# Optimization experiments

Hardware: AMD Instinct MI355X
Metric: run time of the kernel (lower is better)

Reference implementation:

```python
import jax, jax.numpy as jnp
import numpy as np

N_NODES = 50000
N_EDGES = 1600000
D = 128
N_GRAPHS = 512


def _glorot(key, shape):
    fan_in, fan_out = shape[1], shape[0]
    lim = float(np.sqrt(6.0 / (fan_in + fan_out)))
    return jax.random.uniform(key, shape, jnp.float32, -lim, lim)


def setup_inputs() -> dict:
    key = jax.random.key(0)
    ks = jax.random.split(key, 16)
    inp = {
        "x": jax.random.normal(ks[0], (N_NODES, D), jnp.float32),
        "edge_index": jax.random.randint(ks[1], (2, N_EDGES), 0, N_NODES, jnp.int64),
        "batch": jnp.sort(jax.random.randint(ks[2], (N_NODES,), 0, N_GRAPHS, jnp.int64)),
    }
    # 3 SAGEConv layers: W_l (neighbor path, with bias), W_r (root path, no bias)
    for l in range(3):
        inp[f"Wl{l}"] = _glorot(ks[3 + 3 * l], (D, D))
        inp[f"b{l}"] = jnp.zeros((D,), jnp.float32)
        inp[f"Wr{l}"] = _glorot(ks[4 + 3 * l], (D, D))
    inp["fc_w"] = _glorot(ks[14], (1, D))
    inp["fc_b"] = jnp.zeros((1,), jnp.float32)
    return inp


def _sage_layer(x, src, dst, Wl, b, Wr):
    # mean aggregation of source features at destination nodes
    deg = jax.ops.segment_sum(jnp.ones((src.shape[0],), x.dtype), dst, num_segments=N_NODES)
    agg = jax.ops.segment_sum(x[src], dst, num_segments=N_NODES)  # [N, D] gather+scatter
    agg = agg / jnp.clip(deg, 1.0)[:, None]
    return agg @ Wl.T + b + x @ Wr.T


def reference(x, edge_index, batch, Wl0, b0, Wr0, Wl1, b1, Wr1, Wl2, b2, Wr2, fc_w, fc_b):
    src, dst = edge_index[0], edge_index[1]
    for Wl, b, Wr in ((Wl0, b0, Wr0), (Wl1, b1, Wr1), (Wl2, b2, Wr2)):
        x = jax.nn.relu(_sage_layer(x, src, dst, Wl, b, Wr))  # dropout p=0 -> identity
    # global mean pool per graph
    cnt = jax.ops.segment_sum(jnp.ones((x.shape[0],), x.dtype), batch, num_segments=N_GRAPHS)
    pooled = jax.ops.segment_sum(x, batch, num_segments=N_GRAPHS) / jnp.clip(cnt, 1.0)[:, None]
    return pooled @ fc_w.T + fc_b
```

## Files before the change

### kernel.cpp

```cpp
#include <hip/hip_runtime.h>

#define N_NODES  50000
#define N_EDGES  1600000
#define DIM      128
#define N_GRAPHS 512
#define SCAN_BLOCK 1024
#define NB1   196
#define B1    256
#define CHUNK 6250
#define BH_N  (NB1 * B1)
#define BH_BLK ((BH_N + SCAN_BLOCK - 1) / SCAN_BLOCK)
#define XS_BLOCKS 6250
#define WS_BLOCKS 384
#define GB_BLOCKS 196

typedef unsigned int uint_t;
typedef unsigned short ushort_t;
typedef __attribute__((ext_vector_type(8))) short bf16x8;
typedef __attribute__((ext_vector_type(4))) float f32x4;

__device__ inline uint_t bf_rne(float f) {
    uint_t u = __float_as_uint(f);
    return (u + 0x7fffu + ((u >> 16) & 1u)) >> 16;
}

__device__ inline void bf_split(float f, uint_t& h, uint_t& l) {
    h = bf_rne(f);
    float hf = __uint_as_float(h << 16);
    l = bf_rne(f - hf);
}

__global__ __launch_bounds__(256) void prep_kernel(
        const int* __restrict__ dst, int* __restrict__ bh,
        const float* __restrict__ x, ushort_t* __restrict__ xh, ushort_t* __restrict__ xl,
        const float* w0, const float* w1, const float* w2,
        const float* w3, const float* w4, const float* w5,
        ushort_t* __restrict__ whi,
        const int* __restrict__ batch, int* __restrict__ gstart) {
    __shared__ int hist[NB1];
    int b = blockIdx.x, t = threadIdx.x;
    if (b < B1) {
        for (int i = t; i < NB1; i += 256) hist[i] = 0;
        __syncthreads();
        int base = b * CHUNK;
        for (int i = t; i < CHUNK; i += 256)
            atomicAdd(&hist[dst[base + i] >> 8], 1);
        __syncthreads();
        for (int i = t; i < NB1; i += 256) bh[i * B1 + b] = hist[i];
    } else if (b < B1 + XS_BLOCKS) {
        int i = (b - B1) * 256 + t;
        float4 v = ((const float4*)x)[i];
        uint_t h0,h1,h2,h3,l0,l1,l2,l3;
        bf_split(v.x,h0,l0); bf_split(v.y,h1,l1); bf_split(v.z,h2,l2); bf_split(v.w,h3,l3);
        uint2 ho; ho.x = h0 | (h1 << 16); ho.y = h2 | (h3 << 16);
        uint2 lo; lo.x = l0 | (l1 << 16); lo.y = l2 | (l3 << 16);
        ((uint2*)xh)[i] = ho;
        ((uint2*)xl)[i] = lo;
    } else if (b < B1 + XS_BLOCKS + WS_BLOCKS) {
        int i = (b - B1 - XS_BLOCKS) * 256 + t;
        int ws = i >> 14, off = i & 16383;
        const float* w = (ws == 0) ? w0 : (ws == 1) ? w1 : (ws == 2) ? w2
                       : (ws == 3) ? w3 : (ws == 4) ? w4 : w5;
        whi[i] = (ushort_t)bf_rne(w[off]);
    } else {
        int i = (b - B1 - XS_BLOCKS - WS_BLOCKS) * 256 + t;
        if (i < N_NODES) {
            int bb = batch[i];
            int prev = (i == 0) ? -1 : batch[i - 1];
            for (int g = prev + 1; g <= bb; g++) gstart[g] = i;
            if (i == 0) {
                int last = batch[N_NODES - 1];
                for (int g = last + 1; g <= N_GRAPHS; g++) gstart[g] = N_NODES;
            }
        }
    }
}

__global__ void block_reduce_n(const int* __restrict__ in, int* __restrict__ bsum, int n) {
    __shared__ int red[256];
    int b = blockIdx.x, t = threadIdx.x;
    int base = b * SCAN_BLOCK;
    int s = 0;
    for (int i = t; i < SCAN_BLOCK; i += 256) {
        int idx = base + i;
        s += (idx < n) ? in[idx] : 0;
    }
    red[t] = s; __syncthreads();
    for (int off = 128; off; off >>= 1) {
        if (t < off) red[t] += red[t + off];
        __syncthreads();
    }
    if (t == 0) bsum[b] = red[0];
}

__global__ void scan_tops_n(const int* __restrict__ bsum, int* __restrict__ bofs, int nblk) {
    if (threadIdx.x == 0) {
        int acc = 0;
        for (int i = 0; i < nblk; i++) { bofs[i] = acc; acc += bsum[i]; }
    }
}

__global__ void block_scan_n(const int* __restrict__ in, const int* __restrict__ bofs,
                             int* __restrict__ ofs, int n) {
    __shared__ int tmp[SCAN_BLOCK];
    int b = blockIdx.x, t = threadIdx.x;
    int i = b * SCAN_BLOCK + t;
    tmp[t] = (i < n) ? in[i] : 0;
    __syncthreads();
    for (int off = 1; off < SCAN_BLOCK; off <<= 1) {
        int add = (t >= off) ? tmp[t - off] : 0;
        __syncthreads();
        tmp[t] += add;
        __syncthreads();
    }
    if (i < n) ofs[i + 1] = tmp[t] + bofs[b];
    if (i == 0) ofs[0] = 0;
}

__global__ __launch_bounds__(256) void p1_scatter(const int* __restrict__ src,
                                                  const int* __restrict__ dst,
                                                  const int* __restrict__ bhofs,
                                                  uint_t* __restrict__ ebuf1) {
    __shared__ int cur[NB1];
    int b = blockIdx.x, t = threadIdx.x;
    for (int i = t; i < NB1; i += 256) cur[i] = bhofs[i * B1 + b];
    __syncthreads();
    int base = b * CHUNK;
    for (int i = t; i < CHUNK; i += 256) {
        int d = dst[base + i];
        int pos = atomicAdd(&cur[d >> 8], 1);
        ebuf1[pos] = (uint_t)src[base + i] | ((uint_t)(d & 255) << 16);
    }
}

__global__ __launch_bounds__(256) void p2_sort(const uint_t* __restrict__ ebuf1,
                                               const int* __restrict__ bhofs,
                                               int* __restrict__ row_start,
                                               int* __restrict__ ebuf) {
    __shared__ int hist[256];
    __shared__ int scn[256];
    __shared__ int cur[256];
    int k = blockIdx.x, t = threadIdx.x;
    int s = bhofs[k * B1];
    int e = (k == NB1 - 1) ? N_EDGES : bhofs[(k + 1) * B1];
    hist[t] = 0;
    __syncthreads();
    for (int i = s + t; i < e; i += 256)
        atomicAdd(&hist[(ebuf1[i] >> 16) & 255], 1);
    __syncthreads();
    int v = hist[t];
    scn[t] = v;
    __syncthreads();
    for (int off = 1; off < 256; off <<= 1) {
        int add = (t >= off) ? scn[t - off] : 0;
        __syncthreads();
        scn[t] += add;
        __syncthreads();
    }
    int ex = scn[t] - v;
    int node = k * 256 + t;
    if (node < N_NODES) row_start[node] = s + ex;
    if (k == NB1 - 1 && t == 0) row_start[N_NODES] = N_EDGES;
    cur[t] = s + ex;
    __syncthreads();
    for (int i = s + t; i < e; i += 256) {
        uint_t p = ebuf1[i];
        int pos = atomicAdd(&cur[(p >> 16) & 255], 1);
        ebuf[pos] = (int)(p & 0xffffu);
    }
}

__global__ __launch_bounds__(256) void agg_kernel(const ushort_t* __restrict__ xb,
                                                  const int* __restrict__ row_start,
                                                  const int* __restrict__ ebuf,
                                                  ushort_t* __restrict__ agg_hi,
                                                  ushort_t* __restrict__ agg_lo) {
    int node = blockIdx.x * 4 + (threadIdx.x >> 6);
    if (node >= N_NODES) return;
    int lane = threadIdx.x & 63;
    int grp = lane >> 4, fl = lane & 15;
    int s = row_start[node], e = row_start[node + 1];
    float a0=0.f,a1=0.f,a2=0.f,a3=0.f,a4=0.f,a5=0.f,a6=0.f,a7=0.f;
    const uint4* x8 = (const uint4*)xb;
    for (int i = s; i < e; i += 64) {
        int nloc = e - i; if (nloc > 64) nloc = 64;
        int src_l = (i + lane < e) ? ebuf[i + lane] : 0;
        int jmax = (nloc + 3) & ~3;
        #pragma unroll 4
        for (int j = 0; j < jmax; j += 4) {
            int slot = j + grp;
            int src = __shfl(src_l, slot & 63, 64);
            if (slot < nloc) {
                uint4 v = x8[(size_t)src * 16 + fl];
                a0 += __uint_as_float(v.x << 16);
                a1 += __uint_as_float(v.x & 0xffff0000u);
                a2 += __uint_as_float(v.y << 16);
                a3 += __uint_as_float(v.y & 0xffff0000u);
                a4 += __uint_as_float(v.z << 16);
                a5 += __uint_as_float(v.z & 0xffff0000u);
                a6 += __uint_as_float(v.w << 16);
                a7 += __uint_as_float(v.w & 0xffff0000u);
            }
        }
    }
    a0 += __shfl_xor(a0, 16, 64); a0 += __shfl_xor(a0, 32, 64);
    a1 += __shfl_xor(a1, 16, 64); a1 += __shfl_xor(a1, 32, 64);
    a2 += __shfl_xor(a2, 16, 64); a2 += __shfl_xor(a2, 32, 64);
    a3 += __shfl_xor(a3, 16, 64); a3 += __shfl_xor(a3, 32, 64);
    a4 += __shfl_xor(a4, 16, 64); a4 += __shfl_xor(a4, 32, 64);
    a5 += __shfl_xor(a5, 16, 64); a5 += __shfl_xor(a5, 32, 64);
    a6 += __shfl_xor(a6, 16, 64); a6 += __shfl_xor(a6, 32, 64);
    a7 += __shfl_xor(a7, 16, 64); a7 += __shfl_xor(a7, 32, 64);
    if (grp == 0) {
        float inv = (e > s) ? 1.0f / (float)(e - s) : 0.0f;
        float v[8] = {a0*inv,a1*inv,a2*inv,a3*inv,a4*inv,a5*inv,a6*inv,a7*inv};
        uint_t h[8], l[8];
        #pragma unroll
        for (int k = 0; k < 8; k++) bf_split(v[k], h[k], l[k]);
        uint4 ho, lo;
        ho.x = h[0] | (h[1] << 16); ho.y = h[2] | (h[3] << 16);
        ho.z = h[4] | (h[5] << 16); ho.w = h[6] | (h[7] << 16);
        lo.x = l[0] | (l[1] << 16); lo.y = l[2] | (l[3] << 16);
        lo.z = l[4] | (l[5] << 16); lo.w = l[6] | (l[7] << 16);
        ((uint4*)agg_hi)[(size_t)node * 16 + fl] = ho;
        ((uint4*)agg_lo)[(size_t)node * 16 + fl] = lo;
    }
}

__global__ __launch_bounds__(256, 2) void sage_gemm_mfma(
        const ushort_t* __restrict__ agg_hi, const ushort_t* __restrict__ agg_lo,
        const ushort_t* __restrict__ x_hi,   const ushort_t* __restrict__ x_lo,
        const ushort_t* __restrict__ wl_hi,  const ushort_t* __restrict__ wr_hi,
        const float* __restrict__ bias,
        ushort_t* __restrict__ out_hi, ushort_t* __restrict__ out_lo, int nrows) {
    __shared__ ushort_t whi_s[2][16384];
    int t = threadIdx.x;
    for (int i = t; i < 4096; i += 256) {
        int a = i >> 11, rem = i & 2047, row = rem >> 4, ch = rem & 15;
        int sw = ch ^ (row & 7);
        const ushort_t* srcp = a ? wr_hi : wl_hi;
        uint4 v = *(const uint4*)(srcp + row * DIM + ch * 8);
        *(uint4*)((char*)&whi_s[a][0] + row * 256 + sw * 16) = v;
    }
    __syncthreads();

    int wave = t >> 6, lane = t & 63;
    int ml = lane & 15, quad = lane >> 4;
    int m0 = blockIdx.x * 64 + wave * 16;
    int row = m0 + ml;
    int rowc = (row < nrows) ? row : (nrows - 1);
    size_t abase = (size_t)rowc * DIM + quad * 8;

    f32x4 acc[8];
    #pragma unroll
    for (int i = 0; i < 8; i++) acc[i] = (f32x4)0.f;

    #pragma unroll
    for (int kc = 0; kc < DIM; kc += 32) {
        bf16x8 Aah = *(const bf16x8*)(agg_hi + abase + kc);
        bf16x8 Aal = *(const bf16x8*)(agg_lo + abase + kc);
        bf16x8 Axh = *(const bf16x8*)(x_hi   + abase + kc);
        bf16x8 Axl = *(const bf16x8*)(x_lo   + abase + kc);
        int kch = (kc >> 3) + quad;
        int sw16 = (kch ^ (ml & 7)) * 16;
        #pragma unroll
        for (int n0 = 0; n0 < 8; n0++) {
            int nrow = n0 * 16 + ml;
            bf16x8 b_lh = *(const bf16x8*)((const char*)&whi_s[0][0] + nrow * 256 + sw16);
            bf16x8 b_rh = *(const bf16x8*)((const char*)&whi_s[1][0] + nrow * 256 + sw16);
            f32x4 c = acc[n0];
            c = __builtin_amdgcn_mfma_f32_16x16x32_bf16(Aah, b_lh, c, 0, 0, 0);
            c = __builtin_amdgcn_mfma_f32_16x16x32_bf16(Aal, b_lh, c, 0, 0, 0);
            c = __builtin_amdgcn_mfma_f32_16x16x32_bf16(Axh, b_rh, c, 0, 0, 0);
            c = __builtin_amdgcn_mfma_f32_16x16x32_bf16(Axl, b_rh, c, 0, 0, 0);
            acc[n0] = c;
        }
    }

    #pragma unroll
    for (int n0 = 0; n0 < 8; n0++) {
        int col = n0 * 16 + ml;
        float bv = bias[col];
        #pragma unroll
        for (int r = 0; r < 4; r++) {
            int orow = m0 + quad * 4 + r;
            if (orow < nrows) {
                float v = fmaxf(acc[n0][r] + bv, 0.f);
                uint_t h, l;
                bf_split(v, h, l);
                out_hi[(size_t)orow * DIM + col] = (ushort_t)h;
                out_lo[(size_t)orow * DIM + col] = (ushort_t)l;
            }
        }
    }
}

__global__ __launch_bounds__(256) void pool_fc(const ushort_t* __restrict__ x_hi,
                                               const ushort_t* __restrict__ x_lo,
                                               const int* __restrict__ gstart,
                                               const float* __restrict__ fc_w,
                                               const float* __restrict__ fc_b,
                                               float* __restrict__ out) {
    int g = blockIdx.x * 4 + (threadIdx.x >> 6);
    if (g >= N_GRAPHS) return;
    int lane = threadIdx.x & 63;
    int s = gstart[g], e = gstart[g + 1];
    float ax = 0.f, ay = 0.f;
    const uint_t* xh = (const uint_t*)x_hi;
    const uint_t* xl = (const uint_t*)x_lo;
    for (int i = s; i < e; i++) {
        uint_t h = xh[(size_t)i * 64 + lane];
        uint_t l = xl[(size_t)i * 64 + lane];
        ax += __uint_as_float(h << 16) + __uint_as_float(l << 16);
        ay += __uint_as_float(h & 0xffff0000u) + __uint_as_float(l & 0xffff0000u);
    }
    float inv = (e > s) ? 1.0f / (float)(e - s) : 0.0f;
    const float2* w2 = (const float2*)fc_w;
    float2 w = w2[lane];
    float sres = (ax * w.x + ay * w.y) * inv;
    for (int off = 32; off; off >>= 1) sres += __shfl_down(sres, off, 64);
    if (lane == 0) out[g] = sres + fc_b[0];
}

extern "C" void kernel_launch(void* const* d_in, const int* in_sizes, int n_in,
                              void* d_out, int out_size, void* d_ws, size_t ws_size,
                              hipStream_t stream) {
    const float* x     = (const float*)d_in[0];
    const int*   ei    = (const int*)d_in[1];
    const int*   batch = (const int*)d_in[2];
    const float* Wl[3] = {(const float*)d_in[3], (const float*)d_in[6], (const float*)d_in[9]};
    const float* bb[3] = {(const float*)d_in[4], (const float*)d_in[7], (const float*)d_in[10]};
    const float* Wr[3] = {(const float*)d_in[5], (const float*)d_in[8], (const float*)d_in[11]};
    const float* fc_w  = (const float*)d_in[12];
    const float* fc_b  = (const float*)d_in[13];
    float* out = (float*)d_out;

    char* p = (char*)d_ws;
    auto alloc = [&](size_t bytes) { char* r = p; p += (bytes + 255) & ~255ull; return r; };
    int* bh        = (int*)alloc((size_t)BH_N * 4);
    int* bhofs     = (int*)alloc((size_t)(BH_N + 1) * 4);
    int* bsum      = (int*)alloc((size_t)BH_BLK * 4);
    int* bofs      = (int*)alloc((size_t)BH_BLK * 4);
    uint_t* ebuf1  = (uint_t*)alloc((size_t)N_EDGES * 4);
    int* ebuf      = (int*)alloc((size_t)N_EDGES * 4);
    int* row_start = (int*)alloc((size_t)(N_NODES + 1) * 4);
    int* gstart    = (int*)alloc((size_t)(N_GRAPHS + 1) * 4);
    const size_t FB = (size_t)N_NODES * DIM * 2;
    ushort_t* agg_hi = (ushort_t*)alloc(FB);
    ushort_t* agg_lo = (ushort_t*)alloc(FB);
    ushort_t* fh[3]  = {(ushort_t*)alloc(FB), (ushort_t*)alloc(FB), (ushort_t*)alloc(FB)};
    ushort_t* fl_[3] = {(ushort_t*)alloc(FB), (ushort_t*)alloc(FB), (ushort_t*)alloc(FB)};
    ushort_t* whi    = (ushort_t*)alloc((size_t)6 * 16384 * 2);

    const int* src = ei;
    const int* dst = ei + N_EDGES;

    prep_kernel<<<B1 + XS_BLOCKS + WS_BLOCKS + GB_BLOCKS, 256, 0, stream>>>(
        dst, bh, x, fh[0], fl_[0], Wl[0], Wr[0], Wl[1], Wr[1], Wl[2], Wr[2],
        whi, batch, gstart);
    block_reduce_n<<<BH_BLK, 256, 0, stream>>>(bh, bsum, BH_N);
    scan_tops_n<<<1, 64, 0, stream>>>(bsum, bofs, BH_BLK);
    block_scan_n<<<BH_BLK, SCAN_BLOCK, 0, stream>>>(bh, bofs, bhofs, BH_N);
    p1_scatter<<<B1, 256, 0, stream>>>(src, dst, bhofs, ebuf1);
    p2_sort<<<NB1, 256, 0, stream>>>(ebuf1, bhofs, row_start, ebuf);

    int inb = 0;
    for (int l = 0; l < 3; l++) {
        int outb = (l == 0) ? 1 : (l == 1) ? 2 : 1;
        agg_kernel<<<(N_NODES + 3) / 4, 256, 0, stream>>>(fh[inb], row_start, ebuf, agg_hi, agg_lo);
        sage_gemm_mfma<<<(N_NODES + 63) / 64, 256, 0, stream>>>(
            agg_hi, agg_lo, fh[inb], fl_[inb],
            whi + (size_t)(2 * l) * 16384, whi + (size_t)(2 * l + 1) * 16384,
            bb[l], fh[outb], fl_[outb], N_NODES);
        inb = outb;
    }
    pool_fc<<<(N_GRAPHS + 3) / 4, 256, 0, stream>>>(fh[inb], fl_[inb], gstart, fc_w, fc_b, out);
}
```

Baseline: 442.5 us.

## Fuse global mean pool and FC into last GEMM epilogue; merge scan kernels

The last SAGE layer's GEMM epilogue now does bias, ReLU and the dot product with fc_w, reduces across lanes, and atomically adds each row's contribution divided by its graph size into the output. The output is pre-initialised with fc_b in the prep kernel. This removes the final feature-map write and the separate pool_fc kernel. The single-thread top-level scan is also folded into the block scan kernel via a wave shuffle scan, which removes one launch. The cost is atomic contention on 512 outputs and a summation order that is no longer deterministic.

```diff
diff --git a/kernel.cpp b/kernel.cpp
--- a/kernel.cpp
+++ b/kernel.cpp
@@ -13,6 +13,7 @@
 #define XS_BLOCKS 6250
 #define WS_BLOCKS 384
 #define GB_BLOCKS 196
+#define OI_BLOCKS 2
 
 typedef unsigned int uint_t;
 typedef unsigned short ushort_t;
@@ -36,7 +37,8 @@
         const float* w0, const float* w1, const float* w2,
         const float* w3, const float* w4, const float* w5,
         ushort_t* __restrict__ whi,
-        const int* __restrict__ batch, int* __restrict__ gstart) {
+        const int* __restrict__ batch, int* __restrict__ gstart,
+        const float* __restrict__ fc_b, float* __restrict__ out) {
     __shared__ int hist[NB1];
     int b = blockIdx.x, t = threadIdx.x;
     if (b < B1) {
@@ -62,7 +64,7 @@
         const float* w = (ws == 0) ? w0 : (ws == 1) ? w1 : (ws == 2) ? w2
                        : (ws == 3) ? w3 : (ws == 4) ? w4 : w5;
         whi[i] = (ushort_t)bf_rne(w[off]);
-    } else {
+    } else if (b < B1 + XS_BLOCKS + WS_BLOCKS + GB_BLOCKS) {
         int i = (b - B1 - XS_BLOCKS - WS_BLOCKS) * 256 + t;
         if (i < N_NODES) {
             int bb = batch[i];
@@ -73,6 +75,9 @@
                 for (int g = last + 1; g <= N_GRAPHS; g++) gstart[g] = N_NODES;
             }
         }
+    } else {
+        int i = (b - B1 - XS_BLOCKS - WS_BLOCKS - GB_BLOCKS) * 256 + t;
+        if (i < N_GRAPHS) out[i] = fc_b[0];
     }
 }
 
@@ -93,17 +98,21 @@
     if (t == 0) bsum[b] = red[0];
 }
 
-__global__ void scan_tops_n(const int* __restrict__ bsum, int* __restrict__ bofs, int nblk) {
-    if (threadIdx.x == 0) {
-        int acc = 0;
-        for (int i = 0; i < nblk; i++) { bofs[i] = acc; acc += bsum[i]; }
-    }
-}
-
-__global__ void block_scan_n(const int* __restrict__ in, const int* __restrict__ bofs,
-                             int* __restrict__ ofs, int n) {
+__global__ void scan_finalize(const int* __restrict__ in, const int* __restrict__ bsum,
+                              int* __restrict__ ofs, int n, int nblk) {
+    __shared__ int small[64];
     __shared__ int tmp[SCAN_BLOCK];
     int b = blockIdx.x, t = threadIdx.x;
+    if (t < 64) {
+        int v = (t < nblk) ? bsum[t] : 0;
+        for (int off = 1; off < 64; off <<= 1) {
+            int u = __shfl_up(v, off, 64);
+            if (t >= off) v += u;
+        }
+        small[t] = v;
+    }
+    __syncthreads();
+    int base = (b == 0) ? 0 : small[b - 1];
     int i = b * SCAN_BLOCK + t;
     tmp[t] = (i < n) ? in[i] : 0;
     __syncthreads();
@@ -113,7 +122,7 @@
         tmp[t] += add;
         __syncthreads();
     }
-    if (i < n) ofs[i + 1] = tmp[t] + bofs[b];
+    if (i < n) ofs[i + 1] = tmp[t] + base;
     if (i == 0) ofs[0] = 0;
 }
 
@@ -232,7 +241,9 @@
         const ushort_t* __restrict__ x_hi,   const ushort_t* __restrict__ x_lo,
         const ushort_t* __restrict__ wl_hi,  const ushort_t* __restrict__ wr_hi,
         const float* __restrict__ bias,
-        ushort_t* __restrict__ out_hi, ushort_t* __restrict__ out_lo, int nrows) {
+        ushort_t* __restrict__ out_hi, ushort_t* __restrict__ out_lo,
+        const int* __restrict__ batch, const int* __restrict__ gstart,
+        const float* __restrict__ fc_w, float* __restrict__ pool_out, int nrows) {
     __shared__ ushort_t whi_s[2][16384];
     int t = threadIdx.x;
     for (int i = t; i < 4096; i += 256) {
@@ -277,49 +288,47 @@
         }
     }
 
-    #pragma unroll
-    for (int n0 = 0; n0 < 8; n0++) {
-        int col = n0 * 16 + ml;
-        float bv = bias[col];
+    if (pool_out) {
+        float rd[4] = {0.f, 0.f, 0.f, 0.f};
+        #pragma unroll
+        for (int n0 = 0; n0 < 8; n0++) {
+            int col = n0 * 16 + ml;
+            float bv = bias[col];
+            float w  = fc_w[col];
+            #pragma unroll
+            for (int r = 0; r < 4; r++)
+                rd[r] += fmaxf(acc[n0][r] + bv, 0.f) * w;
+        }
         #pragma unroll
         for (int r = 0; r < 4; r++) {
+            #pragma unroll
+            for (int off = 1; off < 16; off <<= 1)
+                rd[r] += __shfl_xor(rd[r], off, 64);
             int orow = m0 + quad * 4 + r;
-            if (orow < nrows) {
-                float v = fmaxf(acc[n0][r] + bv, 0.f);
-                uint_t h, l;
-                bf_split(v, h, l);
-                out_hi[(size_t)orow * DIM + col] = (ushort_t)h;
-                out_lo[(size_t)orow * DIM + col] = (ushort_t)l;
+            if (orow < nrows && ml == 0) {
+                int g = batch[orow];
+                float cnt = (float)(gstart[g + 1] - gstart[g]);
+                atomicAdd(&pool_out[g], rd[r] / cnt);
             }
         }
-    }
-}
-
-__global__ __launch_bounds__(256) void pool_fc(const ushort_t* __restrict__ x_hi,
-                                               const ushort_t* __restrict__ x_lo,
-                                               const int* __restrict__ gstart,
-                                               const float* __restrict__ fc_w,
-                                               const float* __restrict__ fc_b,
-                                               float* __restrict__ out) {
-    int g = blockIdx.x * 4 + (threadIdx.x >> 6);
-    if (g >= N_GRAPHS) return;
-    int lane = threadIdx.x & 63;
-    int s = gstart[g], e = gstart[g + 1];
-    float ax = 0.f, ay = 0.f;
-    const uint_t* xh = (const uint_t*)x_hi;
-    const uint_t* xl = (const uint_t*)x_lo;
-    for (int i = s; i < e; i++) {
-        uint_t h = xh[(size_t)i * 64 + lane];
-        uint_t l = xl[(size_t)i * 64 + lane];
-        ax += __uint_as_float(h << 16) + __uint_as_float(l << 16);
-        ay += __uint_as_float(h & 0xffff0000u) + __uint_as_float(l & 0xffff0000u);
-    }
-    float inv = (e > s) ? 1.0f / (float)(e - s) : 0.0f;
-    const float2* w2 = (const float2*)fc_w;
-    float2 w = w2[lane];
-    float sres = (ax * w.x + ay * w.y) * inv;
-    for (int off = 32; off; off >>= 1) sres += __shfl_down(sres, off, 64);
-    if (lane == 0) out[g] = sres + fc_b[0];
+    } else {
+        #pragma unroll
+        for (int n0 = 0; n0 < 8; n0++) {
+            int col = n0 * 16 + ml;
+            float bv = bias[col];
+            #pragma unroll
+            for (int r = 0; r < 4; r++) {
+                int orow = m0 + quad * 4 + r;
+                if (orow < nrows) {
+                    float v = fmaxf(acc[n0][r] + bv, 0.f);
+                    uint_t h, l;
+                    bf_split(v, h, l);
+                    out_hi[(size_t)orow * DIM + col] = (ushort_t)h;
+                    out_lo[(size_t)orow * DIM + col] = (ushort_t)l;
+                }
+            }
+        }
+    }
 }
 
 extern "C" void kernel_launch(void* const* d_in, const int* in_sizes, int n_in,
@@ -340,7 +349,6 @@
     int* bh        = (int*)alloc((size_t)BH_N * 4);
     int* bhofs     = (int*)alloc((size_t)(BH_N + 1) * 4);
     int* bsum      = (int*)alloc((size_t)BH_BLK * 4);
-    int* bofs      = (int*)alloc((size_t)BH_BLK * 4);
     uint_t* ebuf1  = (uint_t*)alloc((size_t)N_EDGES * 4);
     int* ebuf      = (int*)alloc((size_t)N_EDGES * 4);
     int* row_start = (int*)alloc((size_t)(N_NODES + 1) * 4);
@@ -355,24 +363,23 @@
     const int* src = ei;
     const int* dst = ei + N_EDGES;
 
-    prep_kernel<<<B1 + XS_BLOCKS + WS_BLOCKS + GB_BLOCKS, 256, 0, stream>>>(
+    prep_kernel<<<B1 + XS_BLOCKS + WS_BLOCKS + GB_BLOCKS + OI_BLOCKS, 256, 0, stream>>>(
         dst, bh, x, fh[0], fl_[0], Wl[0], Wr[0], Wl[1], Wr[1], Wl[2], Wr[2],
-        whi, batch, gstart);
+        whi, batch, gstart, fc_b, out);
     block_reduce_n<<<BH_BLK, 256, 0, stream>>>(bh, bsum, BH_N);
-    scan_tops_n<<<1, 64, 0, stream>>>(bsum, bofs, BH_BLK);
-    block_scan_n<<<BH_BLK, SCAN_BLOCK, 0, stream>>>(bh, bofs, bhofs, BH_N);
+    scan_finalize<<<BH_BLK, SCAN_BLOCK, 0, stream>>>(bh, bsum, bhofs, BH_N, BH_BLK);
     p1_scatter<<<B1, 256, 0, stream>>>(src, dst, bhofs, ebuf1);
     p2_sort<<<NB1, 256, 0, stream>>>(ebuf1, bhofs, row_start, ebuf);
 
     int inb = 0;
     for (int l = 0; l < 3; l++) {
-        int outb = (l == 0) ? 1 : (l == 1) ? 2 : 1;
+        int outb = (l == 0) ? 1 : 2;
         agg_kernel<<<(N_NODES + 3) / 4, 256, 0, stream>>>(fh[inb], row_start, ebuf, agg_hi, agg_lo);
         sage_gemm_mfma<<<(N_NODES + 63) / 64, 256, 0, stream>>>(
             agg_hi, agg_lo, fh[inb], fl_[inb],
             whi + (size_t)(2 * l) * 16384, whi + (size_t)(2 * l + 1) * 16384,
-            bb[l], fh[outb], fl_[outb], N_NODES);
+            bb[l], fh[outb], fl_[outb],
+            batch, gstart, fc_w, (l == 2) ? out : (float*)nullptr, N_NODES);
         inb = outb;
     }
-    pool_fc<<<(N_GRAPHS + 3) / 4, 256, 0, stream>>>(fh[inb], fl_[inb], gstart, fc_w, fc_b, out);
-}
+}
```

Measured after the change: 449.9 us. No clear change (+1.7%).
